# Optimization experiments

Hardware: AMD Instinct MI355X
Metric: run time of the kernel (lower is better)

Reference implementation:

```python
import jax, jax.numpy as jnp
import numpy as np

N = 50000          # nodes
E = 800000         # directed edges (before self-loops)
NUM_CLASSES = 10
NEG_SLOPE = 0.2    # PyG GATConv default leaky_relu slope


def segment_softmax(logits, seg, num_segments):
    # numerically stable softmax over edges grouped by target node
    m = jax.ops.segment_max(logits, seg, num_segments=num_segments)
    e = jnp.exp(logits - m[seg])
    s = jax.ops.segment_sum(e, seg, num_segments=num_segments)
    return e / s[seg]


def gat_conv(x, src, dst, W, a_src, a_dst, b, n_nodes):
    # single-head PyG-style GATConv (eval mode: attention dropout disabled)
    h = x @ W                              # [N, C]
    alpha_src = h @ a_src                  # [N]
    alpha_dst = h @ a_dst                  # [N]
    logits = jax.nn.leaky_relu(alpha_src[src] + alpha_dst[dst], NEG_SLOPE)  # [E']
    alpha = segment_softmax(logits, dst, n_nodes)                            # [E']
    out = jax.ops.segment_sum(h[src] * alpha[:, None], dst, num_segments=n_nodes)
    return out + b


def setup_inputs() -> dict:
    key = jax.random.key(0)
    ks = jax.random.split(key, 13)
    x = jax.random.normal(ks[0], (N, 11), dtype=jnp.float32)
    edge_index = jax.random.randint(ks[1], (2, E), 0, N, dtype=jnp.int32)
    batch = jnp.zeros((N,), dtype=jnp.int32)  # unused by forward (no pooling)
    s = 0.1
    W1 = jax.random.normal(ks[2], (11, 16), jnp.float32) * s
    a1_src = jax.random.normal(ks[3], (16,), jnp.float32) * s
    a1_dst = jax.random.normal(ks[4], (16,), jnp.float32) * s
    b1 = jnp.zeros((16,), jnp.float32)
    W2 = jax.random.normal(ks[5], (16, 64), jnp.float32) * s
    a2_src = jax.random.normal(ks[6], (64,), jnp.float32) * s
    a2_dst = jax.random.normal(ks[7], (64,), jnp.float32) * s
    b2 = jnp.zeros((64,), jnp.float32)
    Wl = jax.random.normal(ks[8], (64, NUM_CLASSES), jnp.float32) * s
    bl = jnp.zeros((NUM_CLASSES,), jnp.float32)
    return {"x": x, "edge_index": edge_index, "batch": batch,
            "W1": W1, "a1_src": a1_src, "a1_dst": a1_dst, "b1": b1,
            "W2": W2, "a2_src": a2_src, "a2_dst": a2_dst, "b2": b2,
            "Wl": Wl, "bl": bl}


def reference(x, edge_index, batch, W1, a1_src, a1_dst, b1,
              W2, a2_src, a2_dst, b2, Wl, bl):
    n = x.shape[0]
    loop = jnp.arange(n, dtype=edge_index.dtype)
    src = jnp.concatenate([edge_index[0], loop])  # add self-loops (PyG default)
    dst = jnp.concatenate([edge_index[1], loop])
    h = gat_conv(x, src, dst, W1, a1_src, a1_dst, b1, n)
    h = jax.nn.relu(h)
    h = gat_conv(h, src, dst, W2, a2_src, a2_dst, b2, n)
    return h @ Wl + bl
```

## Files before the change

kernel.cpp:

```cpp
#include <hip/hip_runtime.h>
#include <hip/hip_bf16.h>

#define NEG_SLOPE 0.2f
#define BSTRIDE 8192

__device__ __forceinline__ float lrelu(float x) {
    return x > 0.f ? x : NEG_SLOPE * x;
}

__global__ __launch_bounds__(256)
void front_kernel(const int* __restrict__ ei, int E, int n, int CH,
                  int* __restrict__ bh, int nbuck, int nblk,
                  const float* __restrict__ x,
                  const float* __restrict__ W1,
                  const float* __restrict__ a1s, const float* __restrict__ a1d,
                  float* __restrict__ h, float* __restrict__ as, float* __restrict__ ad,
                  int tb,
                  const float* __restrict__ W2,
                  const float* __restrict__ a2s, const float* __restrict__ a2d,
                  const float* __restrict__ b2,
                  const float* __restrict__ Wl, const float* __restrict__ bl,
                  float* __restrict__ va, float* __restrict__ vd,
                  float* __restrict__ Wc, float* __restrict__ bc,
                  int* __restrict__ gcur) {
    const int bid = blockIdx.x;
    if (bid < nblk) {
        __shared__ int lhist[256];
        for (int i = threadIdx.x; i < nbuck; i += 256) lhist[i] = 0;
        __syncthreads();
        int beg = bid * CH;
        int end = min(beg + CH, E + n);
        for (int e = beg + threadIdx.x; e < end; e += 256) {
            int d = (e < E) ? ei[E + e] : (e - E);
            atomicAdd(&lhist[d >> 8], 1);
        }
        __syncthreads();
        for (int i = threadIdx.x; i < nbuck; i += 256)
            bh[i * nblk + bid] = lhist[i];
    } else if (bid < nblk + tb) {
        constexpr int F_IN = 11, C_OUT = 16;
        __shared__ float sW[F_IN * C_OUT];
        __shared__ float sAs[C_OUT];
        __shared__ float sAd[C_OUT];
        for (int i = threadIdx.x; i < F_IN * C_OUT; i += 256) sW[i] = W1[i];
        if (threadIdx.x < C_OUT) { sAs[threadIdx.x] = a1s[threadIdx.x]; sAd[threadIdx.x] = a1d[threadIdx.x]; }
        __syncthreads();
        int i = (bid - nblk) * 256 + threadIdx.x;
        if (i >= n) return;
        float xin[F_IN];
#pragma unroll
        for (int f = 0; f < F_IN; ++f) xin[f] = x[(size_t)i * F_IN + f];
        float s_acc = 0.f, d_acc = 0.f;
#pragma unroll
        for (int c = 0; c < C_OUT; ++c) {
            float acc = 0.f;
#pragma unroll
            for (int f = 0; f < F_IN; ++f) acc = fmaf(xin[f], sW[f * C_OUT + c], acc);
            h[(size_t)i * C_OUT + c] = acc;
            s_acc = fmaf(acc, sAs[c], s_acc);
            d_acc = fmaf(acc, sAd[c], d_acc);
        }
        as[i] = s_acc;
        ad[i] = d_acc;
    } else {
        int t = threadIdx.x;
        if (t < nbuck) gcur[t] = t * BSTRIDE;
        if (t < 16) {
            float s = 0.f, s2 = 0.f;
            for (int c = 0; c < 64; ++c) {
                float w = W2[t * 64 + c];
                s = fmaf(w, a2s[c], s);
                s2 = fmaf(w, a2d[c], s2);
            }
            va[t] = s; vd[t] = s2;
        }
        int i = t - 64;
        if (i >= 0 && i < 160) {
            int f = i / 10, k = i % 10;
            float s = 0.f;
            for (int c = 0; c < 64; ++c) s = fmaf(W2[f * 64 + c], Wl[c * 10 + k], s);
            Wc[i] = s;
        }
        int k2 = t - 240;
        if (k2 >= 0 && k2 < 10) {
            float s = bl[k2];
            for (int c = 0; c < 64; ++c) s = fmaf(b2[c], Wl[c * 10 + k2], s);
            bc[k2] = s;
        }
    }
}

__global__ void binscatter_kernel(const int* __restrict__ ei, int E, int n, int CH,
                                  const int* __restrict__ bh, int* __restrict__ gcur,
                                  unsigned int* __restrict__ pk, int nbuck, int nblk) {
    __shared__ int lcur[256];
    for (int i = threadIdx.x; i < nbuck; i += blockDim.x) {
        int c = bh[i * nblk + blockIdx.x];
        lcur[i] = (c > 0) ? atomicAdd(&gcur[i], c) : 0;
    }
    __syncthreads();
    int beg = blockIdx.x * CH;
    int end = min(beg + CH, E + n);
    for (int e = beg + threadIdx.x; e < end; e += blockDim.x) {
        int s, d;
        if (e < E) { s = ei[e]; d = ei[E + e]; } else { s = d = e - E; }
        int slot = atomicAdd(&lcur[d >> 8], 1);
        pk[slot] = ((unsigned int)(d & 255) << 24) | (unsigned int)s;
    }
}

__global__ void bucketsort_kernel(const unsigned int* __restrict__ pk,
                                  const int* __restrict__ gcur,
                                  int* __restrict__ csrc,
                                  int* __restrict__ row_beg, int* __restrict__ deg,
                                  int n) {
    __shared__ int lcnt[256];
    __shared__ int lofs[256];
    const int tid = threadIdx.x;
    const int base = blockIdx.x * 256;
    const int beg = blockIdx.x * BSTRIDE;
    const int end = gcur[blockIdx.x];

    lcnt[tid] = 0;
    __syncthreads();
    for (int i = beg + tid; i < end; i += 256)
        atomicAdd(&lcnt[pk[i] >> 24], 1);
    __syncthreads();
    int v = lcnt[tid];
    lofs[tid] = v;
    __syncthreads();
    for (int off = 1; off < 256; off <<= 1) {
        int u = (tid >= off) ? lofs[tid - off] : 0;
        __syncthreads();
        lofs[tid] += u;
        __syncthreads();
    }
    int excl = lofs[tid] - v;
    if (base + tid < n) {
        row_beg[base + tid] = beg + excl;
        deg[base + tid] = v;
    }
    lcnt[tid] = excl;
    __syncthreads();
    for (int i = beg + tid; i < end; i += 256) {
        unsigned int p = pk[i];
        int d = (int)(p >> 24);
        int slot = beg + atomicAdd(&lcnt[d], 1);
        csrc[slot] = (int)(p & 0xFFFFFFu);
    }
}

__global__ void gat_agg1_kernel(const int* __restrict__ row_beg,
                                const int* __restrict__ deg,
                                const int* __restrict__ csrc,
                                const float* __restrict__ as,
                                const float* __restrict__ ad,
                                const float* __restrict__ h,
                                const float* __restrict__ b1,
                                const float* __restrict__ va,
                                const float* __restrict__ vd,
                                float* __restrict__ X1r,
                                float* __restrict__ as2,
                                float* __restrict__ ad2, int n) {
    constexpr int C = 16;
    __shared__ float sb1[16], sva[16], svd[16];
    if (threadIdx.x < 16) {
        sb1[threadIdx.x] = b1[threadIdx.x];
        sva[threadIdx.x] = va[threadIdx.x];
        svd[threadIdx.x] = vd[threadIdx.x];
    }
    __syncthreads();
    int node = (blockIdx.x * blockDim.x + threadIdx.x) >> 4;
    int sl = threadIdx.x & 15;
    if (node >= n) return;
    int beg = row_beg[node];
    int end = beg + deg[node];
    float add = ad[node];

    const int eq = sl >> 2;
    const int cl = sl & 3;
    float lsum = 0.f;
    float4 acc = {0.f, 0.f, 0.f, 0.f};
    for (int chunk = beg; chunk < end; chunk += 16) {
        int e = chunk + sl;
        float wv = 0.f; int sv = 0;
        if (e < end) {
            sv = csrc[e];
            wv = __expf(lrelu(as[sv] + add));
            lsum += wv;
        }
        const int nch = min(16, end - chunk);
        const int T = (nch + 3) >> 2;
        for (int t = 0; t < T; ++t) {
            int j = t * 4 + eq;
            float wj = __shfl(wv, j, 16);
            int   sj = __shfl(sv, j, 16);
            if (j < nch) {
                const float4 hv = *reinterpret_cast<const float4*>(&h[(size_t)sj * C + cl * 4]);
                acc.x = fmaf(wj, hv.x, acc.x);
                acc.y = fmaf(wj, hv.y, acc.y);
                acc.z = fmaf(wj, hv.z, acc.z);
                acc.w = fmaf(wj, hv.w, acc.w);
            }
        }
    }
#pragma unroll
    for (int k = 1; k < 16; k <<= 1) lsum += __shfl_xor(lsum, k, 16);
#pragma unroll
    for (int k = 4; k < 16; k <<= 1) {
        acc.x += __shfl_xor(acc.x, k, 16);
        acc.y += __shfl_xor(acc.y, k, 16);
        acc.z += __shfl_xor(acc.z, k, 16);
        acc.w += __shfl_xor(acc.w, k, 16);
    }
    float inv = 1.f / lsum;
    float x0 = fmaxf(fmaf(acc.x, inv, sb1[cl * 4 + 0]), 0.f);
    float x1 = fmaxf(fmaf(acc.y, inv, sb1[cl * 4 + 1]), 0.f);
    float x2 = fmaxf(fmaf(acc.z, inv, sb1[cl * 4 + 2]), 0.f);
    float x3 = fmaxf(fmaf(acc.w, inv, sb1[cl * 4 + 3]), 0.f);
    if (eq == 0) {
        float4 o = {x0, x1, x2, x3};
        *reinterpret_cast<float4*>(&X1r[(size_t)node * C + cl * 4]) = o;
    }
    float p = x0 * sva[cl * 4] + x1 * sva[cl * 4 + 1] + x2 * sva[cl * 4 + 2] + x3 * sva[cl * 4 + 3];
    float q = x0 * svd[cl * 4] + x1 * svd[cl * 4 + 1] + x2 * svd[cl * 4 + 2] + x3 * svd[cl * 4 + 3];
    p += __shfl_xor(p, 1, 16); p += __shfl_xor(p, 2, 16);
    q += __shfl_xor(q, 1, 16); q += __shfl_xor(q, 2, 16);
    if (sl == 0) { as2[node] = p; ad2[node] = q; }
}

__global__ void gat_agg2_kernel(const int* __restrict__ row_beg,
                                const int* __restrict__ deg,
                                const int* __restrict__ csrc,
                                const float* __restrict__ as2,
                                const float* __restrict__ ad2,
                                const float* __restrict__ X1r,
                                const float* __restrict__ Wc,
                                const float* __restrict__ bc,
                                float* __restrict__ out, int n) {
    constexpr int C = 16;
    __shared__ float sWc[160], sbc[10];
    for (int i = threadIdx.x; i < 160; i += blockDim.x) sWc[i] = Wc[i];
    if (threadIdx.x < 10) sbc[threadIdx.x] = bc[threadIdx.x];
    __syncthreads();
    int node = (blockIdx.x * blockDim.x + threadIdx.x) >> 4;
    int sl = threadIdx.x & 15;
    if (node >= n) return;
    int beg = row_beg[node];
    int end = beg + deg[node];
    float add = ad2[node];

    const int eq = sl >> 2;
    const int cl = sl & 3;
    float lsum = 0.f;
    float4 acc = {0.f, 0.f, 0.f, 0.f};
    for (int chunk = beg; chunk < end; chunk += 16) {
        int e = chunk + sl;
        float wv = 0.f; int sv = 0;
        if (e < end) {
            sv = csrc[e];
            wv = __expf(lrelu(as2[sv] + add));
            lsum += wv;
        }
        const int nch = min(16, end - chunk);
        const int T = (nch + 3) >> 2;
        for (int t = 0; t < T; ++t) {
            int j = t * 4 + eq;
            float wj = __shfl(wv, j, 16);
            int   sj = __shfl(sv, j, 16);
            if (j < nch) {
                const float4 hv = *reinterpret_cast<const float4*>(&X1r[(size_t)sj * C + cl * 4]);
                acc.x = fmaf(wj, hv.x, acc.x);
                acc.y = fmaf(wj, hv.y, acc.y);
                acc.z = fmaf(wj, hv.z, acc.z);
                acc.w = fmaf(wj, hv.w, acc.w);
            }
        }
    }
#pragma unroll
    for (int k = 1; k < 16; k <<= 1) lsum += __shfl_xor(lsum, k, 16);
#pragma unroll
    for (int k = 4; k < 16; k <<= 1) {
        acc.x += __shfl_xor(acc.x, k, 16);
        acc.y += __shfl_xor(acc.y, k, 16);
        acc.z += __shfl_xor(acc.z, k, 16);
        acc.w += __shfl_xor(acc.w, k, 16);
    }
    float inv = 1.f / lsum;
    acc.x *= inv; acc.y *= inv; acc.z *= inv; acc.w *= inv;
    float p[10];
#pragma unroll
    for (int k = 0; k < 10; ++k) {
        p[k] = acc.x * sWc[(cl * 4 + 0) * 10 + k]
             + acc.y * sWc[(cl * 4 + 1) * 10 + k]
             + acc.z * sWc[(cl * 4 + 2) * 10 + k]
             + acc.w * sWc[(cl * 4 + 3) * 10 + k];
    }
#pragma unroll
    for (int k = 0; k < 10; ++k) {
        p[k] += __shfl_xor(p[k], 1, 16);
        p[k] += __shfl_xor(p[k], 2, 16);
    }
    if (sl < 10) {
        float v = p[0];
#pragma unroll
        for (int k = 1; k < 10; ++k) v = (sl == k) ? p[k] : v;
        out[(size_t)node * 10 + sl] = v + sbc[sl];
    }
}

extern "C" void kernel_launch(void* const* d_in, const int* in_sizes, int n_in,
                              void* d_out, int out_size, void* d_ws, size_t ws_size,
                              hipStream_t stream) {
    const float* x       = (const float*)d_in[0];
    const int*   ei      = (const int*)d_in[1];
    const float* W1      = (const float*)d_in[3];
    const float* a1_src  = (const float*)d_in[4];
    const float* a1_dst  = (const float*)d_in[5];
    const float* b1      = (const float*)d_in[6];
    const float* W2      = (const float*)d_in[7];
    const float* a2_src  = (const float*)d_in[8];
    const float* a2_dst  = (const float*)d_in[9];
    const float* b2      = (const float*)d_in[10];
    const float* Wl      = (const float*)d_in[11];
    const float* bl      = (const float*)d_in[12];
    float* out = (float*)d_out;

    const int N = in_sizes[2];
    const int E = in_sizes[1] / 2;
    const int ET = E + N;

    const int B = 256;
    auto cdiv = [](int a, int b) { return (a + b - 1) / b; };

    const int BUCK  = 256;
    const int NBUCK = cdiv(N, BUCK);
    const int NBLK  = 128;
    const int CHB   = cdiv(ET, NBLK);
    const int TB    = cdiv(N, B);

    char* ws = (char*)d_ws;
    size_t off = 0;
    auto alloc = [&](size_t bytes) {
        char* p = ws + off;
        off = (off + bytes + 255) & ~(size_t)255;
        return p;
    };
    float*        h1   = (float*)alloc((size_t)N * 16 * 4);
    float*        X1r  = (float*)alloc((size_t)N * 16 * 4);
    float*        as1  = (float*)alloc((size_t)N * 4);
    float*        ad1  = (float*)alloc((size_t)N * 4);
    float*        as2  = (float*)alloc((size_t)N * 4);
    float*        ad2  = (float*)alloc((size_t)N * 4);
    int*          rowb = (int*)alloc((size_t)N * 4);
    int*          degb = (int*)alloc((size_t)N * 4);
    int*          csrc = (int*)alloc((size_t)NBUCK * BSTRIDE * 4);
    unsigned int* pk   = (unsigned int*)alloc((size_t)NBUCK * BSTRIDE * 4);
    int*          bh   = (int*)alloc((size_t)NBUCK * NBLK * 4);
    int*          gcur = (int*)alloc((size_t)NBUCK * 4);
    float*        va   = (float*)alloc(16 * 4);
    float*        vd   = (float*)alloc(16 * 4);
    float*        Wc   = (float*)alloc(160 * 4);
    float*        bc   = (float*)alloc(10 * 4);
    (void)ws_size;

    front_kernel<<<NBLK + TB + 1, B, 0, stream>>>(
        ei, E, N, CHB, bh, NBUCK, NBLK,
        x, W1, a1_src, a1_dst, h1, as1, ad1, TB,
        W2, a2_src, a2_dst, b2, Wl, bl, va, vd, Wc, bc, gcur);

    binscatter_kernel<<<NBLK, B, 0, stream>>>(ei, E, N, CHB, bh, gcur, pk, NBUCK, NBLK);

    bucketsort_kernel<<<NBUCK, 256, 0, stream>>>(pk, gcur, csrc, rowb, degb, N);

    gat_agg1_kernel<<<cdiv(N * 16, B), B, 0, stream>>>(rowb, degb, csrc, as1, ad1, h1, b1, va, vd, X1r, as2, ad2, N);

    gat_agg2_kernel<<<cdiv(N * 16, B), B, 0, stream>>>(rowb, degb, csrc, as2, ad2, X1r, Wc, bc, out, N);
}
```

Baseline: 77.84 us.

## Fuse histogram into scatter, shrink buckets to 128 and vectorize edge loads

The per-block destination histogram moves out of the front kernel and into the scatter kernel. Each block now builds its local histogram and immediately reserves global slots with atomics on gcur, which removes the bh intermediate array and its extra pass over the destination indices. Buckets shrink from 256 to 128 nodes with a 4096-entry stride, scatter blocks go from 128 to 512, and edge and packed-key reads use int4/uint4 vector loads. The trade-off is that the histogram pass re-reads the destination indices inside scatter. Bucket fill order across blocks also becomes nondeterministic, but correctness does not depend on it since bucketsort re-sorts each bucket.

```diff
diff --git a/kernel.cpp b/kernel.cpp
--- a/kernel.cpp
+++ b/kernel.cpp
@@ -2,42 +2,28 @@
 #include <hip/hip_bf16.h>
 
 #define NEG_SLOPE 0.2f
-#define BSTRIDE 8192
+#define BUCK 128
+#define BSTRIDE 4096
 
 __device__ __forceinline__ float lrelu(float x) {
     return x > 0.f ? x : NEG_SLOPE * x;
 }
 
 __global__ __launch_bounds__(256)
-void front_kernel(const int* __restrict__ ei, int E, int n, int CH,
-                  int* __restrict__ bh, int nbuck, int nblk,
-                  const float* __restrict__ x,
+void front_kernel(const float* __restrict__ x,
                   const float* __restrict__ W1,
                   const float* __restrict__ a1s, const float* __restrict__ a1d,
                   float* __restrict__ h, float* __restrict__ as, float* __restrict__ ad,
-                  int tb,
+                  int n, int tb,
                   const float* __restrict__ W2,
                   const float* __restrict__ a2s, const float* __restrict__ a2d,
                   const float* __restrict__ b2,
                   const float* __restrict__ Wl, const float* __restrict__ bl,
                   float* __restrict__ va, float* __restrict__ vd,
                   float* __restrict__ Wc, float* __restrict__ bc,
-                  int* __restrict__ gcur) {
+                  int* __restrict__ gcur, int nbuck) {
     const int bid = blockIdx.x;
-    if (bid < nblk) {
-        __shared__ int lhist[256];
-        for (int i = threadIdx.x; i < nbuck; i += 256) lhist[i] = 0;
-        __syncthreads();
-        int beg = bid * CH;
-        int end = min(beg + CH, E + n);
-        for (int e = beg + threadIdx.x; e < end; e += 256) {
-            int d = (e < E) ? ei[E + e] : (e - E);
-            atomicAdd(&lhist[d >> 8], 1);
-        }
-        __syncthreads();
-        for (int i = threadIdx.x; i < nbuck; i += 256)
-            bh[i * nblk + bid] = lhist[i];
-    } else if (bid < nblk + tb) {
+    if (bid < tb) {
         constexpr int F_IN = 11, C_OUT = 16;
         __shared__ float sW[F_IN * C_OUT];
         __shared__ float sAs[C_OUT];
@@ -45,7 +31,7 @@
         for (int i = threadIdx.x; i < F_IN * C_OUT; i += 256) sW[i] = W1[i];
         if (threadIdx.x < C_OUT) { sAs[threadIdx.x] = a1s[threadIdx.x]; sAd[threadIdx.x] = a1d[threadIdx.x]; }
         __syncthreads();
-        int i = (bid - nblk) * 256 + threadIdx.x;
+        int i = bid * 256 + threadIdx.x;
         if (i >= n) return;
         float xin[F_IN];
 #pragma unroll
@@ -64,7 +50,7 @@
         ad[i] = d_acc;
     } else {
         int t = threadIdx.x;
-        if (t < nbuck) gcur[t] = t * BSTRIDE;
+        for (int i = t; i < nbuck; i += 256) gcur[i] = i * BSTRIDE;
         if (t < 16) {
             float s = 0.f, s2 = 0.f;
             for (int c = 0; c < 64; ++c) {
@@ -90,63 +76,122 @@
     }
 }
 
-__global__ void binscatter_kernel(const int* __restrict__ ei, int E, int n, int CH,
-                                  const int* __restrict__ bh, int* __restrict__ gcur,
-                                  unsigned int* __restrict__ pk, int nbuck, int nblk) {
-    __shared__ int lcur[256];
-    for (int i = threadIdx.x; i < nbuck; i += blockDim.x) {
-        int c = bh[i * nblk + blockIdx.x];
-        lcur[i] = (c > 0) ? atomicAdd(&gcur[i], c) : 0;
-    }
-    __syncthreads();
-    int beg = blockIdx.x * CH;
-    int end = min(beg + CH, E + n);
-    for (int e = beg + threadIdx.x; e < end; e += blockDim.x) {
-        int s, d;
-        if (e < E) { s = ei[e]; d = ei[E + e]; } else { s = d = e - E; }
-        int slot = atomicAdd(&lcur[d >> 8], 1);
-        pk[slot] = ((unsigned int)(d & 255) << 24) | (unsigned int)s;
-    }
-}
-
-__global__ void bucketsort_kernel(const unsigned int* __restrict__ pk,
-                                  const int* __restrict__ gcur,
-                                  int* __restrict__ csrc,
-                                  int* __restrict__ row_beg, int* __restrict__ deg,
-                                  int n) {
-    __shared__ int lcnt[256];
-    __shared__ int lofs[256];
+__global__ __launch_bounds__(256)
+void scatter_kernel(const int* __restrict__ ei, int E, int n, int CH,
+                    int* __restrict__ gcur, unsigned int* __restrict__ pk, int nbuck) {
+    __shared__ int lhist[512];
+    for (int i = threadIdx.x; i < nbuck; i += 256) lhist[i] = 0;
+    __syncthreads();
+    const int beg = blockIdx.x * CH;
+    const int end = min(beg + CH, E + n);
+    for (int e = beg + threadIdx.x * 4; e < end; e += 1024) {
+        if (e + 3 < E) {
+            const int4 d4 = *reinterpret_cast<const int4*>(&ei[E + e]);
+            atomicAdd(&lhist[d4.x >> 7], 1);
+            atomicAdd(&lhist[d4.y >> 7], 1);
+            atomicAdd(&lhist[d4.z >> 7], 1);
+            atomicAdd(&lhist[d4.w >> 7], 1);
+        } else {
+            for (int k = 0; k < 4 && e + k < end; ++k) {
+                int ee = e + k;
+                int d = (ee < E) ? ei[E + ee] : (ee - E);
+                atomicAdd(&lhist[d >> 7], 1);
+            }
+        }
+    }
+    __syncthreads();
+    for (int i = threadIdx.x; i < nbuck; i += 256) {
+        int c = lhist[i];
+        lhist[i] = (c > 0) ? atomicAdd(&gcur[i], c) : 0;
+    }
+    __syncthreads();
+    for (int e = beg + threadIdx.x * 4; e < end; e += 1024) {
+        if (e + 3 < E) {
+            const int4 s4 = *reinterpret_cast<const int4*>(&ei[e]);
+            const int4 d4 = *reinterpret_cast<const int4*>(&ei[E + e]);
+            int slot;
+            slot = atomicAdd(&lhist[d4.x >> 7], 1);
+            pk[slot] = ((unsigned int)(d4.x & 127) << 25) | (unsigned int)s4.x;
+            slot = atomicAdd(&lhist[d4.y >> 7], 1);
+            pk[slot] = ((unsigned int)(d4.y & 127) << 25) | (unsigned int)s4.y;
+            slot = atomicAdd(&lhist[d4.z >> 7], 1);
+            pk[slot] = ((unsigned int)(d4.z & 127) << 25) | (unsigned int)s4.z;
+            slot = atomicAdd(&lhist[d4.w >> 7], 1);
+            pk[slot] = ((unsigned int)(d4.w & 127) << 25) | (unsigned int)s4.w;
+        } else {
+            for (int k = 0; k < 4 && e + k < end; ++k) {
+                int ee = e + k;
+                int s, d;
+                if (ee < E) { s = ei[ee]; d = ei[E + ee]; } else { s = d = ee - E; }
+                int slot = atomicAdd(&lhist[d >> 7], 1);
+                pk[slot] = ((unsigned int)(d & 127) << 25) | (unsigned int)s;
+            }
+        }
+    }
+}
+
+__global__ __launch_bounds__(256)
+void bucketsort_kernel(const unsigned int* __restrict__ pk,
+                       const int* __restrict__ gcur,
+                       int* __restrict__ csrc,
+                       int* __restrict__ row_beg, int* __restrict__ deg,
+                       int n) {
+    __shared__ int lcnt[BUCK];
+    __shared__ int lofs[BUCK];
     const int tid = threadIdx.x;
-    const int base = blockIdx.x * 256;
+    const int base = blockIdx.x * BUCK;
     const int beg = blockIdx.x * BSTRIDE;
     const int end = gcur[blockIdx.x];
 
-    lcnt[tid] = 0;
-    __syncthreads();
-    for (int i = beg + tid; i < end; i += 256)
-        atomicAdd(&lcnt[pk[i] >> 24], 1);
-    __syncthreads();
-    int v = lcnt[tid];
-    lofs[tid] = v;
-    __syncthreads();
-    for (int off = 1; off < 256; off <<= 1) {
-        int u = (tid >= off) ? lofs[tid - off] : 0;
+    if (tid < BUCK) lcnt[tid] = 0;
+    __syncthreads();
+    for (int i = beg + tid * 4; i < end; i += 1024) {
+        if (i + 3 < end) {
+            const uint4 p4 = *reinterpret_cast<const uint4*>(&pk[i]);
+            atomicAdd(&lcnt[p4.x >> 25], 1);
+            atomicAdd(&lcnt[p4.y >> 25], 1);
+            atomicAdd(&lcnt[p4.z >> 25], 1);
+            atomicAdd(&lcnt[p4.w >> 25], 1);
+        } else {
+            for (int k = 0; k < 4 && i + k < end; ++k)
+                atomicAdd(&lcnt[pk[i + k] >> 25], 1);
+        }
+    }
+    __syncthreads();
+    int v = 0;
+    if (tid < BUCK) { v = lcnt[tid]; lofs[tid] = v; }
+    __syncthreads();
+    for (int off = 1; off < BUCK; off <<= 1) {
+        int u = 0;
+        if (tid < BUCK && tid >= off) u = lofs[tid - off];
         __syncthreads();
-        lofs[tid] += u;
+        if (tid < BUCK && tid >= off) lofs[tid] += u;
         __syncthreads();
     }
-    int excl = lofs[tid] - v;
-    if (base + tid < n) {
-        row_beg[base + tid] = beg + excl;
-        deg[base + tid] = v;
-    }
-    lcnt[tid] = excl;
-    __syncthreads();
-    for (int i = beg + tid; i < end; i += 256) {
-        unsigned int p = pk[i];
-        int d = (int)(p >> 24);
-        int slot = beg + atomicAdd(&lcnt[d], 1);
-        csrc[slot] = (int)(p & 0xFFFFFFu);
+    if (tid < BUCK) {
+        int excl = lofs[tid] - v;
+        if (base + tid < n) {
+            row_beg[base + tid] = beg + excl;
+            deg[base + tid] = v;
+        }
+        lcnt[tid] = excl;
+    }
+    __syncthreads();
+    for (int i = beg + tid * 4; i < end; i += 1024) {
+        if (i + 3 < end) {
+            const uint4 p4 = *reinterpret_cast<const uint4*>(&pk[i]);
+            int slot;
+            slot = beg + atomicAdd(&lcnt[p4.x >> 25], 1); csrc[slot] = (int)(p4.x & 0x1FFFFFFu);
+            slot = beg + atomicAdd(&lcnt[p4.y >> 25], 1); csrc[slot] = (int)(p4.y & 0x1FFFFFFu);
+            slot = beg + atomicAdd(&lcnt[p4.z >> 25], 1); csrc[slot] = (int)(p4.z & 0x1FFFFFFu);
+            slot = beg + atomicAdd(&lcnt[p4.w >> 25], 1); csrc[slot] = (int)(p4.w & 0x1FFFFFFu);
+        } else {
+            for (int k = 0; k < 4 && i + k < end; ++k) {
+                unsigned int p = pk[i + k];
+                int slot = beg + atomicAdd(&lcnt[p >> 25], 1);
+                csrc[slot] = (int)(p & 0x1FFFFFFu);
+            }
+        }
     }
 }
 
@@ -333,10 +378,9 @@
     const int B = 256;
     auto cdiv = [](int a, int b) { return (a + b - 1) / b; };
 
-    const int BUCK  = 256;
     const int NBUCK = cdiv(N, BUCK);
-    const int NBLK  = 128;
-    const int CHB   = cdiv(ET, NBLK);
+    const int NBLK  = 512;
+    const int CHB   = ((cdiv(ET, NBLK) + 3) / 4) * 4;
     const int TB    = cdiv(N, B);
 
     char* ws = (char*)d_ws;
@@ -356,7 +400,6 @@
     int*          degb = (int*)alloc((size_t)N * 4);
     int*          csrc = (int*)alloc((size_t)NBUCK * BSTRIDE * 4);
     unsigned int* pk   = (unsigned int*)alloc((size_t)NBUCK * BSTRIDE * 4);
-    int*          bh   = (int*)alloc((size_t)NBUCK * NBLK * 4);
     int*          gcur = (int*)alloc((size_t)NBUCK * 4);
     float*        va   = (float*)alloc(16 * 4);
     float*        vd   = (float*)alloc(16 * 4);
@@ -364,12 +407,11 @@
     float*        bc   = (float*)alloc(10 * 4);
     (void)ws_size;
 
-    front_kernel<<<NBLK + TB + 1, B, 0, stream>>>(
-        ei, E, N, CHB, bh, NBUCK, NBLK,
-        x, W1, a1_src, a1_dst, h1, as1, ad1, TB,
-        W2, a2_src, a2_dst, b2, Wl, bl, va, vd, Wc, bc, gcur);
-
-    binscatter_kernel<<<NBLK, B, 0, stream>>>(ei, E, N, CHB, bh, gcur, pk, NBUCK, NBLK);
+    front_kernel<<<TB + 1, B, 0, stream>>>(
+        x, W1, a1_src, a1_dst, h1, as1, ad1, N, TB,
+        W2, a2_src, a2_dst, b2, Wl, bl, va, vd, Wc, bc, gcur, NBUCK);
+
+    scatter_kernel<<<NBLK, B, 0, stream>>>(ei, E, N, CHB, gcur, pk, NBUCK);
 
     bucketsort_kernel<<<NBUCK, 256, 0, stream>>>(pk, gcur, csrc, rowb, degb, N);
 
```

Result: faster. 69.83 us (-10.3%).
